# Kernel optimization log

Hardware: AMD Instinct MI355X
Metric: run time of the kernel (lower is better)

The kernel has to match this reference:

```python
import jax, jax.numpy as jnp
import numpy as np

N = 50000
E = 640000
D = 128          # in = hidden = out channels
L = 3            # num_layers
ATT_H = D // 2   # attention hidden width
LN_EPS = 1e-5


def _layer_norm(h, gamma, beta):
    mu = jnp.mean(h, axis=-1, keepdims=True)
    var = jnp.var(h, axis=-1, keepdims=True)
    return (h - mu) * jax.lax.rsqrt(var + LN_EPS) * gamma + beta


def setup_inputs() -> dict:
    key = jax.random.key(0)
    ks = jax.random.split(key, 12)
    x = jax.random.normal(ks[0], (N, D), dtype=jnp.float32)
    edge_index = jax.random.randint(ks[1], (2, E), 0, N, dtype=jnp.int64)
    edge_attr = jax.random.normal(ks[2], (E, 2), dtype=jnp.float32)
    s = 1.0 / np.sqrt(D)
    # Per-layer params stacked on leading L axis (all layers same dims).
    lin_node_w = jax.random.uniform(ks[3], (L, D, D), jnp.float32, -s, s)
    lin_edge_w = jax.random.uniform(ks[4], (L, D + 2, D), jnp.float32, -s, s)
    att_w1 = jax.random.uniform(ks[5], (L, 2 * D, ATT_H), jnp.float32, -s, s)
    att_b1 = jnp.zeros((L, ATT_H), jnp.float32)
    att_w2 = jax.random.uniform(ks[6], (L, ATT_H, 1), jnp.float32, -s, s)
    att_b2 = jnp.zeros((L, 1), jnp.float32)
    bias = jnp.zeros((L, D), jnp.float32)
    ln_gamma = jnp.ones((L, D), jnp.float32)
    ln_beta = jnp.zeros((L, D), jnp.float32)
    return {"x": x, "edge_index": edge_index, "edge_attr": edge_attr,
            "lin_node_w": lin_node_w, "lin_edge_w": lin_edge_w,
            "att_w1": att_w1, "att_b1": att_b1, "att_w2": att_w2,
            "att_b2": att_b2, "bias": bias, "ln_gamma": ln_gamma,
            "ln_beta": ln_beta}


def reference(x, edge_index, edge_attr, lin_node_w, lin_edge_w,
              att_w1, att_b1, att_w2, att_b2, bias, ln_gamma, ln_beta):
    # PyG default flow: x_j = source = edge_index[0], x_i = target = edge_index[1];
    # aggregation ('add') scatters messages into targets. Dropout is a no-op (eval).
    src, dst = edge_index[0], edge_index[1]
    for i in range(L):
        x_input = x
        h = x @ lin_node_w[i]                          # [N, D]
        xj = h[src]                                    # [E, D] gather
        xi = h[dst]                                    # [E, D] gather
        # att(cat(x_i, x_j)) without materializing the concat:
        a1 = jax.nn.relu(xi @ att_w1[i][:D] + xj @ att_w1[i][D:] + att_b1[i])
        att = jax.nn.sigmoid(a1 @ att_w2[i] + att_b2[i])   # [E, 1]
        # lin_edge(cat(x_j, edge_attr)) split the same way:
        msg = att * (xj @ lin_edge_w[i][:D] + edge_attr @ lin_edge_w[i][D:])
        out = jax.ops.segment_sum(msg, dst, num_segments=N) + bias[i]
        out = _layer_norm(out, ln_gamma[i], ln_beta[i])
        if i < L - 1:
            out = jax.nn.relu(out)
        x = out + x_input                              # residual (Identity proj)
    return x
```

## Files before the change

kernel.cpp:

```cpp
#include <hip/hip_runtime.h>
#include <hip/hip_bf16.h>

#define NN 50000
#define EE 640000
#define NB 196

typedef __attribute__((ext_vector_type(8))) short short8;
typedef __attribute__((ext_vector_type(4))) float f32x4;

__device__ __forceinline__ float bf2f(ushort u) {
    return __uint_as_float(((uint)u) << 16);
}
__device__ __forceinline__ ushort f2bf(float f) {
    uint b = __float_as_uint(f);
    uint r = (b + 0x7fffu + ((b >> 16) & 1u)) >> 16;
    return (ushort)r;
}
__device__ __forceinline__ ushort f2bf_rn(float f) {
    return (ushort)((__float_as_uint(f) + 0x8000u) >> 16);
}


__global__ __launch_bounds__(256) void k_hist_compose(
    const int* __restrict__ ei, const float* __restrict__ ea,
    int* __restrict__ counts, uint* __restrict__ eab,
    const float* __restrict__ wn_all, const float* __restrict__ aw1,
    const float* __restrict__ wle, ushort* __restrict__ wcT) {
    if (blockIdx.x < 2500) {
        int e = blockIdx.x * 256 + threadIdx.x;
        if (e < EE) {
            atomicAdd(&counts[ei[EE + e]], 1);
            const float2 v = *(const float2*)(ea + 2 * e);
            eab[e] = ((uint)f2bf(v.y) << 16) | (uint)f2bf(v.x);
        }
        return;
    }
    const int bb = blockIdx.x - 2500;
    const int l = bb >> 7;
    const int k = bb & 127;
    const int t = threadIdx.x;
    const float* wn = wn_all + (l * 128 + k) * 128;
    float acc = 0.f;
    for (int c = 0; c < 128; ++c) {
        float cat;
        if (t < 128)
            cat = aw1[(l * 256 + ((t & 64) << 1) + c) * 64 + (t & 63)];
        else
            cat = wle[(l * 130 + c) * 128 + (t - 128)];
        acc += wn[c] * cat;
    }
    wcT[(l * 256 + t) * 128 + k] = f2bf(acc);
}

__global__ __launch_bounds__(256) void k_scan_a(const int* __restrict__ counts,
                                                int* __restrict__ bsum) {
    int i = blockIdx.x * 256 + threadIdx.x;
    int v = (i < NN) ? counts[i] : 0;
    #pragma unroll
    for (int o = 32; o > 0; o >>= 1) v += __shfl_xor(v, o);
    __shared__ int ws[4];
    if ((threadIdx.x & 63) == 0) ws[threadIdx.x >> 6] = v;
    __syncthreads();
    if (threadIdx.x == 0) bsum[blockIdx.x] = ws[0] + ws[1] + ws[2] + ws[3];
}

__global__ __launch_bounds__(256) void k_scan_b(const int* __restrict__ bsum,
                                                int* __restrict__ boff,
                                                int* __restrict__ offs) {
    const int t = threadIdx.x;
    const int lane = t & 63, wave = t >> 6;
    int v = (t < NB) ? bsum[t] : 0;
    int x = v;
    #pragma unroll
    for (int o = 1; o < 64; o <<= 1) {
        int y = __shfl_up(x, o);
        if (lane >= o) x += y;
    }
    __shared__ int ws[4];
    if (lane == 63) ws[wave] = x;
    __syncthreads();
    int add = 0;
    for (int w = 0; w < wave; ++w) add += ws[w];
    x += add;
    if (t < NB) boff[t] = x - v;
    if (t == 255) offs[NN] = x;
}

__global__ __launch_bounds__(256) void k_scan_c(const int* __restrict__ counts,
                                                const int* __restrict__ boff,
                                                int* __restrict__ offs,
                                                int* __restrict__ cursor) {
    int i = blockIdx.x * 256 + threadIdx.x;
    const int lane = threadIdx.x & 63, wave = threadIdx.x >> 6;
    int v = (i < NN) ? counts[i] : 0;
    int x = v;
    #pragma unroll
    for (int o = 1; o < 64; o <<= 1) {
        int y = __shfl_up(x, o);
        if (lane >= o) x += y;
    }
    __shared__ int ws[4];
    if (lane == 63) ws[wave] = x;
    __syncthreads();
    int add = boff[blockIdx.x];
    for (int w = 0; w < wave; ++w) add += ws[w];
    int ex = add + x - v;
    if (i < NN) {
        offs[i] = ex;
        cursor[i] = ex;
    }
}

__global__ __launch_bounds__(256) void k_scatter(const int* __restrict__ ei,
                                                 int* __restrict__ cursor,
                                                 int* __restrict__ perm) {
    int e = blockIdx.x * 256 + threadIdx.x;
    if (e >= EE) return;
    int d = ei[EE + e];
    int pos = atomicAdd(&cursor[d], 1);
    perm[pos] = e;
}

__global__ __launch_bounds__(256) void k_fill_dst(const int* __restrict__ offs,
                                                  int* __restrict__ csr_dst) {
    int n = blockIdx.x * 256 + threadIdx.x;
    if (n >= NN) return;
    const int b = offs[n], e = offs[n + 1];
    for (int i = b; i < e; ++i) csr_dst[i] = n;
}


#define K1_LOADA(AV, RT)                                                   \
    {                                                                      \
        const float* xrow_ = xin + (size_t)(rbase + (RT) * 16 + lrow) * 128; \
        _Pragma("unroll")                                                  \
        for (int s = 0; s < 4; ++s) {                                      \
            const float* px = xrow_ + s * 32 + kg * 8;                     \
            float4 u = *(const float4*)(px);                               \
            float4 v = *(const float4*)(px + 4);                           \
            short8 av;                                                     \
            av[0] = (short)f2bf(u.x); av[1] = (short)f2bf(u.y);            \
            av[2] = (short)f2bf(u.z); av[3] = (short)f2bf(u.w);            \
            av[4] = (short)f2bf(v.x); av[5] = (short)f2bf(v.y);            \
            av[6] = (short)f2bf(v.z); av[7] = (short)f2bf(v.w);            \
            AV[s] = av;                                                    \
        }                                                                  \
    }

#define K1_COMP(AV, RT)                                                    \
    {                                                                      \
        f32x4 acc[4] = {};                                                 \
        _Pragma("unroll")                                                  \
        for (int t = 0; t < 4; ++t) {                                      \
            _Pragma("unroll")                                              \
            for (int s = 0; s < 4; ++s)                                    \
                acc[t] = __builtin_amdgcn_mfma_f32_16x16x32_bf16(          \
                    AV[s], b[t][s], acc[t], 0, 0, 0);                      \
        }                                                                  \
        _Pragma("unroll")                                                  \
        for (int t = 0; t < 4; ++t) {                                      \
            const int col = c0 + t * 16 + lrow;                            \
            _Pragma("unroll")                                              \
            for (int j = 0; j < 4; ++j)                                    \
                pqr[(size_t)(rbase + (RT) * 16 + kg * 4 + j) * 256 + col] = \
                    f2bf(acc[t][j]);                                       \
        }                                                                  \
    }

__global__ __launch_bounds__(256) void k1_gemm(const float* __restrict__ xin,
                                               const ushort* __restrict__ wcT,
                                               ushort* __restrict__ pqr) {
    const int wave = threadIdx.x >> 6;
    const int lane = threadIdx.x & 63;
    const int rbase = blockIdx.x * 64;
    const int c0 = wave * 64;
    const int lrow = lane & 15;
    const int kg = lane >> 4;

    short8 b[4][4];
    #pragma unroll
    for (int t = 0; t < 4; ++t) {
        const int col = c0 + t * 16 + lrow;
        #pragma unroll
        for (int s = 0; s < 4; ++s)
            b[t][s] = *(const short8*)(wcT + col * 128 + s * 32 + kg * 8);
    }

    if (rbase + 64 <= NN) {
        short8 aA[4], aB[4];
        K1_LOADA(aA, 0)
        K1_LOADA(aB, 1) K1_COMP(aA, 0)
        K1_LOADA(aA, 2) K1_COMP(aB, 1)
        K1_LOADA(aB, 3) K1_COMP(aA, 2)
        K1_COMP(aB, 3)
    } else {
        #pragma unroll
        for (int rt = 0; rt < 4; ++rt) {
            const int r0 = rbase + rt * 16;
            int arow = r0 + lrow;
            if (arow >= NN) arow = NN - 1;
            const float* xrow = xin + (size_t)arow * 128;
            short8 a[4];
            #pragma unroll
            for (int s = 0; s < 4; ++s) {
                const float* px = xrow + s * 32 + kg * 8;
                float4 u = *(const float4*)(px);
                float4 v = *(const float4*)(px + 4);
                short8 av;
                av[0] = (short)f2bf(u.x); av[1] = (short)f2bf(u.y);
                av[2] = (short)f2bf(u.z); av[3] = (short)f2bf(u.w);
                av[4] = (short)f2bf(v.x); av[5] = (short)f2bf(v.y);
                av[6] = (short)f2bf(v.z); av[7] = (short)f2bf(v.w);
                a[s] = av;
            }
            f32x4 acc[4] = {};
            #pragma unroll
            for (int t = 0; t < 4; ++t) {
                #pragma unroll
                for (int s = 0; s < 4; ++s)
                    acc[t] = __builtin_amdgcn_mfma_f32_16x16x32_bf16(a[s], b[t][s], acc[t], 0, 0, 0);
            }
            #pragma unroll
            for (int t = 0; t < 4; ++t) {
                const int col = c0 + t * 16 + lrow;
                #pragma unroll
                for (int j = 0; j < 4; ++j) {
                    const int orow = r0 + kg * 4 + j;
                    if (orow < NN)
                        pqr[(size_t)orow * 256 + col] = f2bf(acc[t][j]);
                }
            }
        }
    }
}


__global__ __launch_bounds__(256) void k_att(
    int first, const int* __restrict__ perm, const int* __restrict__ ei,
    const uint* __restrict__ eab, const int* __restrict__ csr_dst,
    uint2* __restrict__ adjSE, float* __restrict__ attv,
    const ushort* __restrict__ pqr, const float* __restrict__ b1v,
    const float* __restrict__ w2v, const float* __restrict__ b2v) {
    const int lane = threadIdx.x & 63;
    const int e0 = blockIdx.x * 256 + (threadIdx.x >> 6) * 64;
    const int row = lane & 15;
    const int kg = lane >> 4;
    const float b2 = b2v[0];

    short8 bv0, bv1;
    const bool col0 = (row == 0);
    #pragma unroll
    for (int j = 0; j < 8; ++j) {
        bv0[j] = (short)f2bf(col0 ? w2v[kg * 8 + j] : 0.f);
        bv1[j] = (short)f2bf(col0 ? w2v[32 + kg * 8 + j] : 0.f);
    }

    uint srcs[4], dsts[4];
    if (first) {
        #pragma unroll
        for (int t = 0; t < 4; ++t) {
            const int pos = e0 + t * 16 + row;
            const int e = perm[pos];
            const uint s = (uint)ei[e];
            srcs[t] = s;
            dsts[t] = (uint)csr_dst[pos];
            adjSE[pos] = make_uint2(s, eab[e]);
        }
    } else {
        #pragma unroll
        for (int t = 0; t < 4; ++t) {
            const int pos = e0 + t * 16 + row;
            srcs[t] = adjSE[pos].x;
            dsts[t] = (uint)csr_dst[pos];
        }
    }

    f32x4 acc[4] = {};
    #pragma unroll
    for (int h = 0; h < 2; ++h) {
        const int cb = 32 * h + kg * 8;
        float4 bA = *(const float4*)(b1v + cb);
        float4 bB = *(const float4*)(b1v + cb + 4);
        const short8 bfrag = h ? bv1 : bv0;
        #pragma unroll
        for (int t = 0; t < 4; ++t) {
            short8 qv = *(const short8*)(pqr + (size_t)srcs[t] * 256 + 64 + cb);
            short8 pv = *(const short8*)(pqr + (size_t)dsts[t] * 256 + cb);
            short8 av;
            #pragma unroll
            for (int j = 0; j < 8; ++j) {
                float bb = (j < 4) ? ((const float*)&bA)[j] : ((const float*)&bB)[j - 4];
                float v = bf2f((ushort)qv[j]) + bf2f((ushort)pv[j]) + bb;
                av[j] = (short)f2bf_rn(fmaxf(v, 0.f));
            }
            acc[t] = __builtin_amdgcn_mfma_f32_16x16x32_bf16(av, bfrag, acc[t], 0, 0, 0);
        }
    }
    if (row == 0) {
        #pragma unroll
        for (int t = 0; t < 4; ++t) {
            float4 o;
            #pragma unroll
            for (int j = 0; j < 4; ++j) {
                float s = acc[t][j] + b2;
                ((float*)&o)[j] = 1.f / (1.f + __expf(-s));
            }
            *(float4*)(attv + e0 + t * 16 + kg * 4) = o;
        }
    }
}


#define CONS(MM, AA, RR, JJ)                                          \
    {                                                                 \
        const float a_ = ((JJ) < ee) ? (AA) : 0.f;                    \
        acc0 = fmaf(a_, __uint_as_float((RR) << 16), acc0);           \
        acc1 = fmaf(a_, __uint_as_float((RR) & 0xffff0000u), acc1);   \
        sE0  = fmaf(a_, __uint_as_float((MM).y << 16), sE0);          \
        sE1  = fmaf(a_, __uint_as_float((MM).y & 0xffff0000u), sE1);  \
    }

#define LOADQ(M0, M1, M2, M3, A0, A1, A2, A3, R0, R1, R2, R3, BASE)  \
    {                                                                \
        M0 = adjSE[(BASE)];                                          \
        M1 = adjSE[(BASE) + 1];                                      \
        M2 = adjSE[(BASE) + 2];                                      \
        M3 = adjSE[(BASE) + 3];                                      \
        A0 = attv[(BASE)];                                           \
        A1 = attv[(BASE) + 1];                                       \
        A2 = attv[(BASE) + 2];                                       \
        A3 = attv[(BASE) + 3];                                       \
        R0 = *(const uint*)(rp + (size_t)M0.x * 256);                \
        R1 = *(const uint*)(rp + (size_t)M1.x * 256);                \
        R2 = *(const uint*)(rp + (size_t)M2.x * 256);                \
        R3 = *(const uint*)(rp + (size_t)M3.x * 256);                \
    }

__global__ __launch_bounds__(256) void k_msg(
    const int* __restrict__ offs, const uint2* __restrict__ adjSE,
    const float* __restrict__ attv, const ushort* __restrict__ pqr,
    const float* __restrict__ xin, const float* __restrict__ web,
    const float* __restrict__ biasv, const float* __restrict__ gammav,
    const float* __restrict__ betav, float* __restrict__ xout, int do_relu) {
    const int lane = threadIdx.x & 63;
    const int n = blockIdx.x * 4 + (threadIdx.x >> 6);
    const int c0 = 2 * lane;

    const int eb = __builtin_amdgcn_readfirstlane(offs[n]);
    const int ee = __builtin_amdgcn_readfirstlane(offs[n + 1]);

    float acc0 = 0.f, acc1 = 0.f, sE0 = 0.f, sE1 = 0.f;
    if (eb < ee) {
        const ushort* rp = pqr + 128 + c0;
        uint2 a0, a1, a2, a3, b0, b1, b2, b3;
        float fa0, fa1, fa2, fa3, fb0, fb1, fb2, fb3;
        uint ra0, ra1, ra2, ra3, rb0, rb1, rb2, rb3;
        LOADQ(a0, a1, a2, a3, fa0, fa1, fa2, fa3, ra0, ra1, ra2, ra3, eb);
        LOADQ(b0, b1, b2, b3, fb0, fb1, fb2, fb3, rb0, rb1, rb2, rb3, eb + 4);
        int j = eb;
        for (; j + 8 < ee; j += 8) {
            CONS(a0, fa0, ra0, j) CONS(a1, fa1, ra1, j + 1)
            CONS(a2, fa2, ra2, j + 2) CONS(a3, fa3, ra3, j + 3)
            LOADQ(a0, a1, a2, a3, fa0, fa1, fa2, fa3, ra0, ra1, ra2, ra3, j + 8);
            CONS(b0, fb0, rb0, j + 4) CONS(b1, fb1, rb1, j + 5)
            CONS(b2, fb2, rb2, j + 6) CONS(b3, fb3, rb3, j + 7)
            LOADQ(b0, b1, b2, b3, fb0, fb1, fb2, fb3, rb0, rb1, rb2, rb3, j + 12);
        }
        CONS(a0, fa0, ra0, j) CONS(a1, fa1, ra1, j + 1)
        CONS(a2, fa2, ra2, j + 2) CONS(a3, fa3, ra3, j + 3)
        CONS(b0, fb0, rb0, j + 4) CONS(b1, fb1, rb1, j + 5)
        CONS(b2, fb2, rb2, j + 6) CONS(b3, fb3, rb3, j + 7)
    }

    const float web00 = web[c0], web01 = web[c0 + 1];
    const float web10 = web[128 + c0], web11 = web[128 + c0 + 1];
    acc0 += sE0 * web00 + sE1 * web10;
    acc1 += sE0 * web01 + sE1 * web11;

    const float2 bi = *(const float2*)(biasv + c0);
    float v0 = acc0 + bi.x;
    float v1 = acc1 + bi.y;
    float sm = v0 + v1, sq = v0 * v0 + v1 * v1;
    #pragma unroll
    for (int o = 32; o > 0; o >>= 1) {
        sm += __shfl_xor(sm, o);
        sq += __shfl_xor(sq, o);
    }
    const float mean = sm * (1.f / 128.f);
    const float var = sq * (1.f / 128.f) - mean * mean;
    const float inv = rsqrtf(var + 1e-5f);
    const float2 ga = *(const float2*)(gammav + c0);
    const float2 be = *(const float2*)(betav + c0);
    float y0 = (v0 - mean) * inv * ga.x + be.x;
    float y1 = (v1 - mean) * inv * ga.y + be.y;
    if (do_relu) { y0 = fmaxf(y0, 0.f); y1 = fmaxf(y1, 0.f); }
    const float2 xr = *(const float2*)(xin + (size_t)n * 128 + c0);
    y0 += xr.x;
    y1 += xr.y;
    float2 o2; o2.x = y0; o2.y = y1;
    *(float2*)(xout + (size_t)n * 128 + c0) = o2;
}


extern "C" void kernel_launch(void* const* d_in, const int* in_sizes, int n_in,
                              void* d_out, int out_size, void* d_ws, size_t ws_size,
                              hipStream_t stream) {
    const float* x   = (const float*)d_in[0];
    const int*   ei  = (const int*)d_in[1];
    const float* ea  = (const float*)d_in[2];
    const float* wn  = (const float*)d_in[3];
    const float* wle = (const float*)d_in[4];
    const float* aw1 = (const float*)d_in[5];
    const float* ab1 = (const float*)d_in[6];
    const float* aw2 = (const float*)d_in[7];
    const float* ab2 = (const float*)d_in[8];
    const float* bia = (const float*)d_in[9];
    const float* gam = (const float*)d_in[10];
    const float* bet = (const float*)d_in[11];

    char* w = (char*)d_ws;
    size_t o = 0;
    auto alloc = [&](size_t bytes) {
        char* p = w + o;
        o = (o + bytes + 255) & ~(size_t)255;
        return p;
    };
    int*    counts  = (int*)alloc((size_t)NN * 4);
    int*    offs    = (int*)alloc((size_t)(NN + 1) * 4);
    int*    cursor  = (int*)alloc((size_t)NN * 4);
    int*    bsum    = (int*)alloc((size_t)NB * 4);
    int*    boff    = (int*)alloc((size_t)NB * 4);
    int*    perm    = (int*)alloc((size_t)EE * 4);
    int*    csr_dst = (int*)alloc((size_t)EE * 4);
    uint*   eab     = (uint*)alloc((size_t)EE * 4);
    uint2*  adjSE   = (uint2*)alloc((size_t)(EE + 64) * 8);
    float*  attv    = (float*)alloc((size_t)(EE + 64) * 4);
    ushort* wcT     = (ushort*)alloc((size_t)3 * 256 * 128 * 2);
    ushort* pqr     = (ushort*)alloc((size_t)NN * 256 * 2);
    float*  xb1     = (float*)alloc((size_t)NN * 128 * 4);
    float*  xb2     = (float*)alloc((size_t)NN * 128 * 4);

    hipMemsetAsync(counts, 0, (size_t)NN * 4, stream);
    hipMemsetAsync(adjSE + EE, 0, (size_t)64 * 8, stream);
    hipMemsetAsync(attv + EE, 0, (size_t)64 * 4, stream);
    k_hist_compose<<<2500 + 384, 256, 0, stream>>>(ei, ea, counts, eab,
                                                   wn, aw1, wle, wcT);
    k_scan_a<<<NB, 256, 0, stream>>>(counts, bsum);
    k_scan_b<<<1, 256, 0, stream>>>(bsum, boff, offs);
    k_scan_c<<<NB, 256, 0, stream>>>(counts, boff, offs, cursor);
    k_scatter<<<(EE + 255) / 256, 256, 0, stream>>>(ei, cursor, perm);
    k_fill_dst<<<NB, 256, 0, stream>>>(offs, csr_dst);

    const float* xi = x;
    float* xo = xb1;
    for (int l = 0; l < 3; ++l) {
        k1_gemm<<<(NN + 63) / 64, 256, 0, stream>>>(xi, wcT + (size_t)l * 256 * 128, pqr);
        k_att<<<EE / 256, 256, 0, stream>>>(l == 0 ? 1 : 0, perm, ei, eab, csr_dst,
                                            adjSE, attv, pqr,
                                            ab1 + l * 64, aw2 + l * 64, ab2 + l);
        const bool last = (l == 2);
        float* out_ptr = last ? (float*)d_out : xo;
        k_msg<<<NN / 4, 256, 0, stream>>>(
            offs, adjSE, attv, pqr, xi,
            wle + ((size_t)l * 130 + 128) * 128,
            bia + l * 128, gam + l * 128, bet + l * 128,
            out_ptr, last ? 0 : 1);
        xi = out_ptr;
        xo = (l == 0) ? xb2 : xb1;
    }
}
```

Before: 351.9 us.

## Replace global-atomic CSR build with two-level bucket sort using shared-memory atomics

Rebuilds the destination-sorted edge list with a two-pass bucket sort. Edges are first binned into 256-node buckets using per-block shared-memory histograms, a scan, and a staged scatter. Each bucket is then sorted locally in shared memory, which writes adjSE, csr_dst and offs directly. This replaces per-node global atomics, the multi-kernel scan, the perm indirection and the serial fill_dst loop, and it removes the first-layer gather path from k_att. The cost is an extra staged buffer pass. Edge order within a node is nondeterministic, which can change float summation order.

```diff
diff --git a/kernel.cpp b/kernel.cpp
--- a/kernel.cpp
+++ b/kernel.cpp
@@ -3,7 +3,9 @@
 
 #define NN 50000
 #define EE 640000
-#define NB 196
+#define ABLK 625
+#define AEDG 1024
+#define NBK 196
 
 typedef __attribute__((ext_vector_type(8))) short short8;
 typedef __attribute__((ext_vector_type(4))) float f32x4;
@@ -21,23 +23,155 @@
 }
 
 
-__global__ __launch_bounds__(256) void k_hist_compose(
-    const int* __restrict__ ei, const float* __restrict__ ea,
-    int* __restrict__ counts, uint* __restrict__ eab,
-    const float* __restrict__ wn_all, const float* __restrict__ aw1,
-    const float* __restrict__ wle, ushort* __restrict__ wcT) {
-    if (blockIdx.x < 2500) {
-        int e = blockIdx.x * 256 + threadIdx.x;
-        if (e < EE) {
-            atomicAdd(&counts[ei[EE + e]], 1);
-            const float2 v = *(const float2*)(ea + 2 * e);
-            eab[e] = ((uint)f2bf(v.y) << 16) | (uint)f2bf(v.x);
+__global__ __launch_bounds__(256) void k_bucketA(const int* __restrict__ ei,
+                                                 const float* __restrict__ ea,
+                                                 uint* __restrict__ eab,
+                                                 int* __restrict__ bcnt) {
+    __shared__ int h[NBK];
+    const int t = threadIdx.x;
+    for (int i = t; i < NBK; i += 256) h[i] = 0;
+    __syncthreads();
+    const int base = blockIdx.x * AEDG;
+    #pragma unroll
+    for (int k = 0; k < 4; ++k) {
+        const int e = base + k * 256 + t;
+        const int d = ei[EE + e];
+        atomicAdd(&h[d >> 8], 1);
+        const float2 v = *(const float2*)(ea + 2 * e);
+        eab[e] = ((uint)f2bf(v.y) << 16) | (uint)f2bf(v.x);
+    }
+    __syncthreads();
+    for (int i = t; i < NBK; i += 256)
+        bcnt[i * ABLK + blockIdx.x] = h[i];
+}
+
+
+__global__ __launch_bounds__(256) void k_scanbkt(const int* __restrict__ bcnt,
+                                                 int* __restrict__ boff2,
+                                                 int* __restrict__ tot) {
+    const int b = blockIdx.x;
+    const int t = threadIdx.x;
+    const int lane = t & 63, wv = t >> 6;
+    __shared__ int ws[4];
+    int run = 0;
+    for (int k = 0; k < 3; ++k) {
+        const int j = k * 256 + t;
+        const int v = (j < ABLK) ? bcnt[b * ABLK + j] : 0;
+        int x = v;
+        #pragma unroll
+        for (int o = 1; o < 64; o <<= 1) {
+            int y = __shfl_up(x, o);
+            if (lane >= o) x += y;
         }
-        return;
-    }
-    const int bb = blockIdx.x - 2500;
-    const int l = bb >> 7;
-    const int k = bb & 127;
+        if (lane == 63) ws[wv] = x;
+        __syncthreads();
+        int add = 0;
+        for (int w = 0; w < wv; ++w) add += ws[w];
+        if (j < ABLK) boff2[b * ABLK + j] = run + add + x - v;
+        const int btot = ws[0] + ws[1] + ws[2] + ws[3];
+        __syncthreads();
+        run += btot;
+    }
+    if (t == 0) tot[b] = run;
+}
+
+
+__global__ __launch_bounds__(256) void k_scantot(const int* __restrict__ tot,
+                                                 int* __restrict__ bbase) {
+    const int t = threadIdx.x;
+    const int lane = t & 63, wv = t >> 6;
+    const int v = (t < NBK) ? tot[t] : 0;
+    int x = v;
+    #pragma unroll
+    for (int o = 1; o < 64; o <<= 1) {
+        int y = __shfl_up(x, o);
+        if (lane >= o) x += y;
+    }
+    __shared__ int ws[4];
+    if (lane == 63) ws[wv] = x;
+    __syncthreads();
+    int add = 0;
+    for (int w = 0; w < wv; ++w) add += ws[w];
+    if (t < NBK) bbase[t] = add + x - v;
+    if (t == 255) bbase[NBK] = add + x;
+}
+
+
+__global__ __launch_bounds__(256) void k_bucketB(const int* __restrict__ ei,
+                                                 const uint* __restrict__ eab,
+                                                 const int* __restrict__ bbase,
+                                                 const int* __restrict__ boff2,
+                                                 uint2* __restrict__ staged) {
+    __shared__ int cur[NBK];
+    const int t = threadIdx.x;
+    for (int i = t; i < NBK; i += 256)
+        cur[i] = bbase[i] + boff2[i * ABLK + blockIdx.x];
+    __syncthreads();
+    const int base = blockIdx.x * AEDG;
+    #pragma unroll
+    for (int k = 0; k < 4; ++k) {
+        const int e = base + k * 256 + t;
+        const int d = ei[EE + e];
+        const uint s = (uint)ei[e];
+        const int pos = atomicAdd(&cur[d >> 8], 1);
+        staged[pos] = make_uint2(s | ((uint)(d & 255) << 20), eab[e]);
+    }
+}
+
+
+__global__ __launch_bounds__(256) void k_bucketC(const int* __restrict__ bbase,
+                                                 const uint2* __restrict__ staged,
+                                                 uint2* __restrict__ adjSE,
+                                                 int* __restrict__ offs,
+                                                 int* __restrict__ csr_dst) {
+    const int b = blockIdx.x;
+    const int t = threadIdx.x;
+    const int lane = t & 63, wv = t >> 6;
+    const int sbeg = bbase[b], send = bbase[b + 1];
+
+    __shared__ int cnt[256];
+    __shared__ int cur[256];
+    __shared__ int ws[4];
+    cnt[t] = 0;
+    __syncthreads();
+    for (int i = sbeg + t; i < send; i += 256)
+        atomicAdd(&cnt[(staged[i].x >> 20) & 255], 1);
+    __syncthreads();
+
+    const int v = cnt[t];
+    int x = v;
+    #pragma unroll
+    for (int o = 1; o < 64; o <<= 1) {
+        int y = __shfl_up(x, o);
+        if (lane >= o) x += y;
+    }
+    if (lane == 63) ws[wv] = x;
+    __syncthreads();
+    int add = 0;
+    for (int w = 0; w < wv; ++w) add += ws[w];
+    const int excl = add + x - v;
+
+    const int node = b * 256 + t;
+    if (node <= NN) offs[node] = sbeg + excl;
+    cur[t] = sbeg + excl;
+    __syncthreads();
+
+    for (int i = sbeg + t; i < send; i += 256) {
+        const uint2 r = staged[i];
+        const int din = (r.x >> 20) & 255;
+        const int pos = atomicAdd(&cur[din], 1);
+        adjSE[pos] = make_uint2(r.x & 0xFFFFFu, r.y);
+        csr_dst[pos] = b * 256 + din;
+    }
+}
+
+
+__global__ __launch_bounds__(256) void k_compose(const float* __restrict__ wn_all,
+                                                 const float* __restrict__ aw1,
+                                                 const float* __restrict__ wle,
+                                                 ushort* __restrict__ wcT) {
+    const int l = blockIdx.x >> 7;
+    const int k = blockIdx.x & 127;
     const int t = threadIdx.x;
     const float* wn = wn_all + (l * 128 + k) * 128;
     float acc = 0.f;
@@ -50,83 +184,6 @@
         acc += wn[c] * cat;
     }
     wcT[(l * 256 + t) * 128 + k] = f2bf(acc);
-}
-
-__global__ __launch_bounds__(256) void k_scan_a(const int* __restrict__ counts,
-                                                int* __restrict__ bsum) {
-    int i = blockIdx.x * 256 + threadIdx.x;
-    int v = (i < NN) ? counts[i] : 0;
-    #pragma unroll
-    for (int o = 32; o > 0; o >>= 1) v += __shfl_xor(v, o);
-    __shared__ int ws[4];
-    if ((threadIdx.x & 63) == 0) ws[threadIdx.x >> 6] = v;
-    __syncthreads();
-    if (threadIdx.x == 0) bsum[blockIdx.x] = ws[0] + ws[1] + ws[2] + ws[3];
-}
-
-__global__ __launch_bounds__(256) void k_scan_b(const int* __restrict__ bsum,
-                                                int* __restrict__ boff,
-                                                int* __restrict__ offs) {
-    const int t = threadIdx.x;
-    const int lane = t & 63, wave = t >> 6;
-    int v = (t < NB) ? bsum[t] : 0;
-    int x = v;
-    #pragma unroll
-    for (int o = 1; o < 64; o <<= 1) {
-        int y = __shfl_up(x, o);
-        if (lane >= o) x += y;
-    }
-    __shared__ int ws[4];
-    if (lane == 63) ws[wave] = x;
-    __syncthreads();
-    int add = 0;
-    for (int w = 0; w < wave; ++w) add += ws[w];
-    x += add;
-    if (t < NB) boff[t] = x - v;
-    if (t == 255) offs[NN] = x;
-}
-
-__global__ __launch_bounds__(256) void k_scan_c(const int* __restrict__ counts,
-                                                const int* __restrict__ boff,
-                                                int* __restrict__ offs,
-                                                int* __restrict__ cursor) {
-    int i = blockIdx.x * 256 + threadIdx.x;
-    const int lane = threadIdx.x & 63, wave = threadIdx.x >> 6;
-    int v = (i < NN) ? counts[i] : 0;
-    int x = v;
-    #pragma unroll
-    for (int o = 1; o < 64; o <<= 1) {
-        int y = __shfl_up(x, o);
-        if (lane >= o) x += y;
-    }
-    __shared__ int ws[4];
-    if (lane == 63) ws[wave] = x;
-    __syncthreads();
-    int add = boff[blockIdx.x];
-    for (int w = 0; w < wave; ++w) add += ws[w];
-    int ex = add + x - v;
-    if (i < NN) {
-        offs[i] = ex;
-        cursor[i] = ex;
-    }
-}
-
-__global__ __launch_bounds__(256) void k_scatter(const int* __restrict__ ei,
-                                                 int* __restrict__ cursor,
-                                                 int* __restrict__ perm) {
-    int e = blockIdx.x * 256 + threadIdx.x;
-    if (e >= EE) return;
-    int d = ei[EE + e];
-    int pos = atomicAdd(&cursor[d], 1);
-    perm[pos] = e;
-}
-
-__global__ __launch_bounds__(256) void k_fill_dst(const int* __restrict__ offs,
-                                                  int* __restrict__ csr_dst) {
-    int n = blockIdx.x * 256 + threadIdx.x;
-    if (n >= NN) return;
-    const int b = offs[n], e = offs[n + 1];
-    for (int i = b; i < e; ++i) csr_dst[i] = n;
 }
 
 
@@ -236,11 +293,10 @@
 
 
 __global__ __launch_bounds__(256) void k_att(
-    int first, const int* __restrict__ perm, const int* __restrict__ ei,
-    const uint* __restrict__ eab, const int* __restrict__ csr_dst,
-    uint2* __restrict__ adjSE, float* __restrict__ attv,
-    const ushort* __restrict__ pqr, const float* __restrict__ b1v,
-    const float* __restrict__ w2v, const float* __restrict__ b2v) {
+    const uint2* __restrict__ adjSE, const int* __restrict__ csr_dst,
+    float* __restrict__ attv, const ushort* __restrict__ pqr,
+    const float* __restrict__ b1v, const float* __restrict__ w2v,
+    const float* __restrict__ b2v) {
     const int lane = threadIdx.x & 63;
     const int e0 = blockIdx.x * 256 + (threadIdx.x >> 6) * 64;
     const int row = lane & 15;
@@ -256,23 +312,11 @@
     }
 
     uint srcs[4], dsts[4];
-    if (first) {
-        #pragma unroll
-        for (int t = 0; t < 4; ++t) {
-            const int pos = e0 + t * 16 + row;
-            const int e = perm[pos];
-            const uint s = (uint)ei[e];
-            srcs[t] = s;
-            dsts[t] = (uint)csr_dst[pos];
-            adjSE[pos] = make_uint2(s, eab[e]);
-        }
-    } else {
-        #pragma unroll
-        for (int t = 0; t < 4; ++t) {
-            const int pos = e0 + t * 16 + row;
-            srcs[t] = adjSE[pos].x;
-            dsts[t] = (uint)csr_dst[pos];
-        }
+    #pragma unroll
+    for (int t = 0; t < 4; ++t) {
+        const int pos = e0 + t * 16 + row;
+        srcs[t] = adjSE[pos].x;
+        dsts[t] = (uint)csr_dst[pos];
     }
 
     f32x4 acc[4] = {};
@@ -425,14 +469,14 @@
         o = (o + bytes + 255) & ~(size_t)255;
         return p;
     };
-    int*    counts  = (int*)alloc((size_t)NN * 4);
     int*    offs    = (int*)alloc((size_t)(NN + 1) * 4);
-    int*    cursor  = (int*)alloc((size_t)NN * 4);
-    int*    bsum    = (int*)alloc((size_t)NB * 4);
-    int*    boff    = (int*)alloc((size_t)NB * 4);
-    int*    perm    = (int*)alloc((size_t)EE * 4);
+    int*    bcnt    = (int*)alloc((size_t)NBK * ABLK * 4);
+    int*    boff2   = (int*)alloc((size_t)NBK * ABLK * 4);
+    int*    tot     = (int*)alloc((size_t)NBK * 4);
+    int*    bbase   = (int*)alloc((size_t)(NBK + 1) * 4);
+    uint*   eab     = (uint*)alloc((size_t)EE * 4);
+    uint2*  staged  = (uint2*)alloc((size_t)EE * 8);
     int*    csr_dst = (int*)alloc((size_t)EE * 4);
-    uint*   eab     = (uint*)alloc((size_t)EE * 4);
     uint2*  adjSE   = (uint2*)alloc((size_t)(EE + 64) * 8);
     float*  attv    = (float*)alloc((size_t)(EE + 64) * 4);
     ushort* wcT     = (ushort*)alloc((size_t)3 * 256 * 128 * 2);
@@ -440,23 +484,20 @@
     float*  xb1     = (float*)alloc((size_t)NN * 128 * 4);
     float*  xb2     = (float*)alloc((size_t)NN * 128 * 4);
 
-    hipMemsetAsync(counts, 0, (size_t)NN * 4, stream);
     hipMemsetAsync(adjSE + EE, 0, (size_t)64 * 8, stream);
     hipMemsetAsync(attv + EE, 0, (size_t)64 * 4, stream);
-    k_hist_compose<<<2500 + 384, 256, 0, stream>>>(ei, ea, counts, eab,
-                                                   wn, aw1, wle, wcT);
-    k_scan_a<<<NB, 256, 0, stream>>>(counts, bsum);
-    k_scan_b<<<1, 256, 0, stream>>>(bsum, boff, offs);
-    k_scan_c<<<NB, 256, 0, stream>>>(counts, boff, offs, cursor);
-    k_scatter<<<(EE + 255) / 256, 256, 0, stream>>>(ei, cursor, perm);
-    k_fill_dst<<<NB, 256, 0, stream>>>(offs, csr_dst);
+    k_bucketA<<<ABLK, 256, 0, stream>>>(ei, ea, eab, bcnt);
+    k_compose<<<384, 256, 0, stream>>>(wn, aw1, wle, wcT);
+    k_scanbkt<<<NBK, 256, 0, stream>>>(bcnt, boff2, tot);
+    k_scantot<<<1, 256, 0, stream>>>(tot, bbase);
+    k_bucketB<<<ABLK, 256, 0, stream>>>(ei, eab, bbase, boff2, staged);
+    k_bucketC<<<NBK, 256, 0, stream>>>(bbase, staged, adjSE, offs, csr_dst);
 
     const float* xi = x;
     float* xo = xb1;
     for (int l = 0; l < 3; ++l) {
         k1_gemm<<<(NN + 63) / 64, 256, 0, stream>>>(xi, wcT + (size_t)l * 256 * 128, pqr);
-        k_att<<<EE / 256, 256, 0, stream>>>(l == 0 ? 1 : 0, perm, ei, eab, csr_dst,
-                                            adjSE, attv, pqr,
+        k_att<<<EE / 256, 256, 0, stream>>>(adjSE, csr_dst, attv, pqr,
                                             ab1 + l * 64, aw2 + l * 64, ab2 + l);
         const bool last = (l == 2);
         float* out_ptr = last ? (float*)d_out : xo;
```

After: 295.4 us. 1.19x faster.
